# Optimization experiments

Measured on AMD Instinct MI355X. Metric: run time of the kernel, lower is better.

Reference implementation:

```python
import jax, jax.numpy as jnp
import numpy as np

N = 20000      # nodes
E = 640000     # edges
DIN = 92       # atom feature dim
C = 128        # hidden_dim
H = 2          # GAT heads
LAYERS = 2     # shared-weight layer count
BN_EPS = 1e-5


def _bn(x, gamma, beta):
    # BatchNorm1d in training mode: batch statistics over the node axis
    mu = x.mean(0)
    var = x.var(0)
    return (x - mu) * jax.lax.rsqrt(var + BN_EPS) * gamma + beta


def _segment_softmax(logits, seg, num_segments):
    # logits: [E', H], seg: [E'] destination ids; softmax per destination node
    m = jax.ops.segment_max(logits, seg, num_segments=num_segments)
    ex = jnp.exp(logits - m[seg])
    s = jax.ops.segment_sum(ex, seg, num_segments=num_segments)
    return ex / s[seg]


def setup_inputs() -> dict:
    key = jax.random.key(0)
    ks = jax.random.split(key, 16)
    def w(k, shape, fan_in):
        return (jax.random.normal(k, shape, jnp.float32) / np.sqrt(fan_in)).astype(jnp.float32)
    return {
        "node_features_s": jax.random.normal(ks[0], (N, DIN), jnp.float32),
        "edge_index_s": jax.random.randint(ks[1], (2, E), 0, N, dtype=jnp.int64),
        "eps_noise": jax.random.normal(ks[2], (N, C), jnp.float32),
        # atom_emb: Linear(DIN,C) + BN + ReLU
        "W_emb": w(ks[3], (DIN, C), DIN), "b_emb": jnp.zeros((C,), jnp.float32),
        "g_emb": jnp.ones((C,), jnp.float32), "be_emb": jnp.zeros((C,), jnp.float32),
        # GIN MLP (shared across all enc layers): Linear+BN+ReLU+Linear
        "W1": w(ks[4], (C, C), C), "b1": jnp.zeros((C,), jnp.float32),
        "g1": jnp.ones((C,), jnp.float32), "be1": jnp.zeros((C,), jnp.float32),
        "W2": w(ks[5], (C, C), C), "b2": jnp.zeros((C,), jnp.float32),
        # VAE heads
        "W_mu": w(ks[6], (C, C), C), "b_mu": jnp.zeros((C,), jnp.float32),
        "W_var": w(ks[7], (C, C), C), "b_var": jnp.zeros((C,), jnp.float32),
        # GAT (shared across all dec layers): lin -> [N,H,C], attention vecs, bias
        "W_gat": w(ks[8], (C, H * C), C),
        "att_src": w(ks[9], (H, C), C), "att_dst": w(ks[10], (H, C), C),
        "b_gat": jnp.zeros((H * C,), jnp.float32),
        # decoder Linear(H*C, C)
        "W_dec": w(ks[11], (H * C, C), H * C), "b_dec": jnp.zeros((C,), jnp.float32),
    }


def reference(node_features_s, edge_index_s, eps_noise,
              W_emb, b_emb, g_emb, be_emb,
              W1, b1, g1, be1, W2, b2,
              W_mu, b_mu, W_var, b_var,
              W_gat, att_src, att_dst, b_gat,
              W_dec, b_dec):
    src, dst = edge_index_s[0], edge_index_s[1]

    # atom embedding
    x = jax.nn.relu(_bn(node_features_s @ W_emb + b_emb, g_emb, be_emb))

    # GIN encoder (eps=0, sum aggregation), shared weights across layers
    for _ in range(LAYERS):
        agg = jax.ops.segment_sum(x[src], dst, num_segments=N)
        h = x + agg
        h = jax.nn.relu(_bn(h @ W1 + b1, g1, be1))
        x = h @ W2 + b2

    mu = x @ W_mu + b_mu
    logvar = x @ W_var + b_var
    z = eps_noise * jnp.exp(0.5 * logvar) + mu
    zin = z

    # GAT decoder with self-loops (PyG default), shared weights
    loop = jnp.arange(N, dtype=src.dtype)
    src_sl = jnp.concatenate([src, loop])
    dst_sl = jnp.concatenate([dst, loop])
    zout = z
    for _ in range(LAYERS):
        hh = (zout @ W_gat).reshape(N, H, C)            # [N,H,C]
        a_s = jnp.einsum('nhc,hc->nh', hh, att_src)     # [N,H]
        a_d = jnp.einsum('nhc,hc->nh', hh, att_dst)
        logits = jax.nn.leaky_relu(a_s[src_sl] + a_d[dst_sl], 0.2)  # [E',H]
        alpha = _segment_softmax(logits, dst_sl, N)
        msg = alpha[:, :, None] * hh[src_sl]            # [E',H,C]
        out = jax.ops.segment_sum(msg, dst_sl, num_segments=N)      # [N,H,C]
        out = out.reshape(N, H * C) + b_gat
        zout = out @ W_dec + b_dec

    return (zin, zout, mu, logvar)
```

## Files before the change

### kernel.cpp

```cpp
#include <hip/hip_runtime.h>
#include <hip/hip_bf16.h>

#define NN   20000
#define DIN_ 92
#define CC   128
#define EE   640000
#define CAP  128
#define BN_EPS 1e-5f

typedef short short8 __attribute__((ext_vector_type(8)));
typedef float floatx4 __attribute__((ext_vector_type(4)));

static __device__ __forceinline__ float b2f(__hip_bfloat16 v) { return __bfloat162float(v); }
static __device__ __forceinline__ float ldf(const void* p, int i, int f32) {
    return f32 ? ((const float*)p)[i]
               : __bfloat162float(((const __hip_bfloat16*)p)[i]);
}
static __device__ __forceinline__ void stf(void* p, int i, float v, int f32) {
    if (f32) ((float*)p)[i] = v;
    else     ((__hip_bfloat16*)p)[i] = __float2bfloat16(v);
}
static __device__ __forceinline__ float leaky02(float x) { return x > 0.f ? x : 0.2f * x; }

static __device__ __forceinline__ float2 bfp(unsigned w) {
    return make_float2(__uint_as_float(w << 16), __uint_as_float(w & 0xffff0000u));
}
static __device__ __forceinline__ float4 bf4(unsigned x, unsigned y) {
    return make_float4(__uint_as_float(x << 16), __uint_as_float(x & 0xffff0000u),
                       __uint_as_float(y << 16), __uint_as_float(y & 0xffff0000u));
}
static __device__ __forceinline__ uint2 f4bf(float4 v) {
    union { uint2 u; __hip_bfloat16 b[4]; } x;
    x.b[0] = __float2bfloat16(v.x); x.b[1] = __float2bfloat16(v.y);
    x.b[2] = __float2bfloat16(v.z); x.b[3] = __float2bfloat16(v.w);
    return x.u;
}
static __device__ __forceinline__ unsigned f2bf(float2 v) {
    union { unsigned u; __hip_bfloat16 b[2]; } x;
    x.b[0] = __float2bfloat16(v.x); x.b[1] = __float2bfloat16(v.y);
    return x.u;
}
static __device__ __forceinline__ short bf16s(float v) {
    union { __hip_bfloat16 b; unsigned short u; } cv;
    cv.b = __float2bfloat16(v);
    return (short)cv.u;
}

#define R0_ 12288
#define R1_ (R0_ + 16384)
#define R2_ (R1_ + 16384)
#define R3_ (R2_ + 16384)
#define R4_ (R3_ + 16384)
#define R5_ (R4_ + 32768)
#define R6_ (R5_ + 32768)
#define TCVT (R6_ + NN * 96)
#define CHUNK 2048
#define NCH ((EE + CHUNK - 1) / CHUNK)
#define HB (NCH * 8)
#define CVTB ((TCVT + 255) / 256)

__global__ __launch_bounds__(256) void cvt_scatter_kernel(
    const void* __restrict__ w_emb, const void* __restrict__ w1,
    const void* __restrict__ w2, const void* __restrict__ wmu,
    const void* __restrict__ wvar, const void* __restrict__ wgat,
    const void* __restrict__ wdec, const void* __restrict__ xin,
    const unsigned* __restrict__ ei,
    __hip_bfloat16* __restrict__ dst,
    int* __restrict__ flags, int* __restrict__ deg,
    unsigned short* __restrict__ csr)
{
    if ((int)blockIdx.x < HB) {
        __shared__ int cz;
        if (threadIdx.x == 0) cz = 0;
        __syncthreads();
        if (ei[2 * threadIdx.x + 1] == 0u) atomicAdd(&cz, 1);
        __syncthreads();
        const int i64 = (cz >= 250);
        int r = blockIdx.x & 7;
        int c = blockIdx.x >> 3;
        int base = c * CHUNK + threadIdx.x;
#pragma unroll
        for (int k = 0; k < CHUNK / 256; k++) {
            int e = base + k * 256;
            if (e < EE) {
                int d = i64 ? (int)((const long long*)ei)[EE + e] : ((const int*)ei)[EE + e];
                if (d / 2500 == r) {
                    int s = i64 ? (int)((const long long*)ei)[e] : ((const int*)ei)[e];
                    int pos = atomicAdd(&deg[d], 1);
                    if (pos < CAP) csr[(d << 7) + pos] = (unsigned short)s;
                }
            }
        }
        return;
    }

    __shared__ int cnt_band, cnt_zero;
    if (threadIdx.x == 0) { cnt_band = 0; cnt_zero = 0; }
    __syncthreads();
    {
        unsigned wv = ((const unsigned*)xin)[threadIdx.x];
        unsigned eb = ((wv & 0xFFFFu) >> 7) & 0xFFu;
        if (eb >= 90u && eb <= 140u) atomicAdd(&cnt_band, 1);
        if ((int)blockIdx.x == HB && ei[2 * threadIdx.x + 1] == 0u) atomicAdd(&cnt_zero, 1);
    }
    __syncthreads();
    const int f32 = (cnt_band < 200) ? 1 : 0;
    if ((int)blockIdx.x == HB && threadIdx.x == 0) {
        flags[0] = f32;
        flags[1] = (cnt_zero >= 250) ? 1 : 0;
    }

    int i = ((int)blockIdx.x - HB) * 256 + threadIdx.x;
    if (i >= TCVT) return;
    float v;
    if (i < R0_) {
        int n = i / 96, k = i - n * 96;
        v = (k < DIN_) ? ldf(w_emb, k * 128 + n, f32) : 0.f;
    } else if (i < R1_) {
        int j = i - R0_; int n = j >> 7, k = j & 127; v = ldf(w1, k * 128 + n, f32);
    } else if (i < R2_) {
        int j = i - R1_; int n = j >> 7, k = j & 127; v = ldf(w2, k * 128 + n, f32);
    } else if (i < R3_) {
        int j = i - R2_; int n = j >> 7, k = j & 127; v = ldf(wmu, k * 128 + n, f32);
    } else if (i < R4_) {
        int j = i - R3_; int n = j >> 7, k = j & 127; v = ldf(wvar, k * 128 + n, f32);
    } else if (i < R5_) {
        int j = i - R4_; int n = j >> 7, k = j & 127; v = ldf(wgat, k * 256 + n, f32);
    } else if (i < R6_) {
        int j = i - R5_; int n = j >> 8, k = j & 255; v = ldf(wdec, k * 128 + n, f32);
    } else {
        int j = i - R6_; int row = j / 96, k = j - row * 96;
        v = (k < DIN_) ? ldf(xin, row * DIN_ + k, f32) : 0.f;
    }
    dst[i] = __float2bfloat16(v);
}

template<int KP, int NC, int CG, int OUT_MODE, int STATS, int BN_A>
__global__ __launch_bounds__(256) void mfma_gemm_kernel(
    const __hip_bfloat16* __restrict__ A,
    const __hip_bfloat16* __restrict__ WT,
    const void* __restrict__ bias,
    void* __restrict__ Cout, int out_off, float* __restrict__ part,
    const float* __restrict__ bnsums, const void* __restrict__ bng,
    const void* __restrict__ bnbe, const int* __restrict__ flags)
{
    const int f32 = flags[0];
    constexpr int MB = 16 * (4 / CG);
    constexpr int CT = NC / (16 * CG);
    __shared__ float sc_s[128], sh_s[128];
    if (BN_A) {
        int t = threadIdx.x;
        if (t < 128) {
            float mean = bnsums[t] * (1.f / NN);
            float var  = bnsums[128 + t] * (1.f / NN) - mean * mean;
            float rs   = rsqrtf(fmaxf(var, 0.f) + BN_EPS);
            float g    = ldf(bng, t, f32);
            float sc   = rs * g;
            sc_s[t] = sc;
            sh_s[t] = ldf(bnbe, t, f32) - mean * sc;
        }
        __syncthreads();
    }
    int w = threadIdx.x >> 6, l = threadIdx.x & 63;
    int rt = w / CG, cg = w - rt * CG;
    int m0 = blockIdx.x * MB + rt * 16;
    int n0 = cg * (16 * CT);
    int l15 = l & 15, kq = (l >> 4) * 8;
    const __hip_bfloat16* arow = A + (size_t)(m0 + l15) * KP + kq;

    floatx4 acc[CT];
#pragma unroll
    for (int ct = 0; ct < CT; ct++) acc[ct] = (floatx4){0.f, 0.f, 0.f, 0.f};

    for (int kc = 0; kc < KP / 32; kc++) {
        short8 a = *(const short8*)(arow + kc * 32);
        if (BN_A) {
#pragma unroll
            for (int k = 0; k < 8; k++) {
                int c = kq + kc * 32 + k;
                float v = __uint_as_float(((unsigned)(unsigned short)a[k]) << 16);
                float o = v * sc_s[c] + sh_s[c];
                a[k] = bf16s(o > 0.f ? o : 0.f);
            }
        }
#pragma unroll
        for (int ct = 0; ct < CT; ct++) {
            const __hip_bfloat16* brow = WT + (size_t)(n0 + ct * 16 + l15) * KP + kq;
            short8 b = *(const short8*)(brow + kc * 32);
            acc[ct] = __builtin_amdgcn_mfma_f32_16x16x32_bf16(a, b, acc[ct], 0, 0, 0);
        }
    }

    int quad = l >> 4;
#pragma unroll
    for (int ct = 0; ct < CT; ct++) {
        int col = n0 + ct * 16 + l15;
        float bb = bias ? ldf(bias, col, f32) : 0.f;
        float sl = 0.f, ql = 0.f;
#pragma unroll
        for (int r = 0; r < 4; r++) {
            int row = m0 + quad * 4 + r;
            float v = acc[ct][r] + bb;
            size_t o = (size_t)row * NC + col;
            if (OUT_MODE == 0)      ((float*)Cout)[o] = v;
            else if (OUT_MODE == 1) ((__hip_bfloat16*)Cout)[o] = __float2bfloat16(v);
            else                    stf(Cout, out_off + (int)o, v, f32);
            if (STATS) { sl += v; ql += v * v; }
        }
        if (STATS) {
            sl += __shfl_xor(sl, 16); sl += __shfl_xor(sl, 32);
            ql += __shfl_xor(ql, 16); ql += __shfl_xor(ql, 32);
            if (quad == 0) {
                part[blockIdx.x * 512 + rt * 256 + col] = sl;
                part[blockIdx.x * 512 + rt * 256 + 128 + col] = ql;
            }
        }
    }
}

__global__ void bn_reduce_kernel(const float* __restrict__ part, float* __restrict__ sums,
                                 int nblk)
{
    int c = threadIdx.x;
    int per = (nblk + (int)gridDim.x - 1) / (int)gridDim.x;
    int b0 = blockIdx.x * per;
    int b1 = min(b0 + per, nblk);
    float v = 0.f;
    for (int b = b0; b < b1; b++)
        v += part[b * 512 + c] + part[b * 512 + 256 + c];
    atomicAdd(&sums[c], v);
}

__global__ __launch_bounds__(256) void gemm_zatt_kernel(
    const __hip_bfloat16* __restrict__ A, const __hip_bfloat16* __restrict__ WTmuv,
    const __hip_bfloat16* __restrict__ WTgat,
    const void* __restrict__ eps, const void* __restrict__ b_mu, const void* __restrict__ b_var,
    __hip_bfloat16* __restrict__ HH,
    const void* __restrict__ attS, const void* __restrict__ attD,
    float* __restrict__ AS, float* __restrict__ AD,
    void* __restrict__ out, const int* __restrict__ flags)
{
    const int f32 = flags[0];
    __shared__ float zs[16][257];
    __shared__ __hip_bfloat16 zb[16][136];
    __shared__ float sS[4][16], sD[4][16];
    int w = threadIdx.x >> 6, l = threadIdx.x & 63;
    int m0 = blockIdx.x * 16;
    int n0 = w * 64;
    int l15 = l & 15, quad = l >> 4, kq = quad * 8;
    const __hip_bfloat16* arow = A + (size_t)(m0 + l15) * 128 + kq;

    floatx4 acc[4];
#pragma unroll
    for (int ct = 0; ct < 4; ct++) acc[ct] = (floatx4){0.f, 0.f, 0.f, 0.f};
    for (int kc = 0; kc < 4; kc++) {
        short8 a = *(const short8*)(arow + kc * 32);
#pragma unroll
        for (int ct = 0; ct < 4; ct++) {
            const __hip_bfloat16* brow = WTmuv + (size_t)(n0 + ct * 16 + l15) * 128 + kq;
            short8 b = *(const short8*)(brow + kc * 32);
            acc[ct] = __builtin_amdgcn_mfma_f32_16x16x32_bf16(a, b, acc[ct], 0, 0, 0);
        }
    }
#pragma unroll
    for (int ct = 0; ct < 4; ct++) {
#pragma unroll
        for (int r = 0; r < 4; r++)
            zs[quad * 4 + r][n0 + ct * 16 + l15] = acc[ct][r];
    }
    __syncthreads();
    int t = threadIdx.x;
    const int NB2 = NN * CC;
#pragma unroll
    for (int k = 0; k < 8; k++) {
        int idx = k * 256 + t;
        int row = idx >> 7, c = idx & 127;
        float mu = zs[row][c]       + ldf(b_mu,  c, f32);
        float lv = zs[row][128 + c] + ldf(b_var, c, f32);
        int gi = (m0 + row) * 128 + c;
        float z = ldf(eps, gi, f32) * expf(0.5f * lv) + mu;
        zb[row][c] = __float2bfloat16(z);
        stf(out, gi, z, f32);
        stf(out, 2 * NB2 + gi, mu, f32);
        stf(out, 3 * NB2 + gi, lv, f32);
    }
    __syncthreads();

    int h = w >> 1;
    floatx4 acc2[4];
#pragma unroll
    for (int ct = 0; ct < 4; ct++) acc2[ct] = (floatx4){0.f, 0.f, 0.f, 0.f};
    for (int kc = 0; kc < 4; kc++) {
        short8 a = *(const short8*)(&zb[l15][kq + kc * 32]);
#pragma unroll
        for (int ct = 0; ct < 4; ct++) {
            const __hip_bfloat16* brow = WTgat + (size_t)(n0 + ct * 16 + l15) * 128 + kq;
            short8 b = *(const short8*)(brow + kc * 32);
            acc2[ct] = __builtin_amdgcn_mfma_f32_16x16x32_bf16(a, b, acc2[ct], 0, 0, 0);
        }
    }
    float spart[4] = {0.f, 0.f, 0.f, 0.f};
    float dpart[4] = {0.f, 0.f, 0.f, 0.f};
#pragma unroll
    for (int ct = 0; ct < 4; ct++) {
        int col = n0 + ct * 16 + l15;
        int cm  = col - 128 * h;
        float as_w = ldf(attS, h * CC + cm, f32);
        float ad_w = ldf(attD, h * CC + cm, f32);
#pragma unroll
        for (int r = 0; r < 4; r++) {
            float v = acc2[ct][r];
            HH[(size_t)(m0 + quad * 4 + r) * 256 + col] = __float2bfloat16(v);
            spart[r] += v * as_w;
            dpart[r] += v * ad_w;
        }
    }
#pragma unroll
    for (int o = 1; o <= 8; o <<= 1) {
#pragma unroll
        for (int r = 0; r < 4; r++) {
            spart[r] += __shfl_xor(spart[r], o);
            dpart[r] += __shfl_xor(dpart[r], o);
        }
    }
    if (l15 == 0) {
#pragma unroll
        for (int r = 0; r < 4; r++) {
            sS[w][quad * 4 + r] = spart[r];
            sD[w][quad * 4 + r] = dpart[r];
        }
    }
    __syncthreads();
    if (t < 32) {
        int row = t & 15, hh2 = t >> 4;
        AS[(m0 + row) * 2 + hh2] = sS[2 * hh2][row] + sS[2 * hh2 + 1][row];
        AD[(m0 + row) * 2 + hh2] = sD[2 * hh2][row] + sD[2 * hh2 + 1][row];
    }
}

__global__ __launch_bounds__(256) void gemm_decatt_kernel(
    const __hip_bfloat16* __restrict__ A, const __hip_bfloat16* __restrict__ WTdec,
    const __hip_bfloat16* __restrict__ WTgat, const void* __restrict__ b_dec,
    __hip_bfloat16* __restrict__ HH,
    const void* __restrict__ attS, const void* __restrict__ attD,
    float* __restrict__ AS, float* __restrict__ AD, const int* __restrict__ flags)
{
    const int f32 = flags[0];
    __shared__ __hip_bfloat16 zo[32][136];
    int w = threadIdx.x >> 6, l = threadIdx.x & 63;
    int rt = w >> 1, cg = w & 1;
    int l15 = l & 15, quad = l >> 4, kq = quad * 8;
    int m0 = blockIdx.x * 32;

    {
        int n0 = cg * 64;
        const __hip_bfloat16* arow = A + (size_t)(m0 + rt * 16 + l15) * 256 + kq;
        floatx4 acc[4];
#pragma unroll
        for (int ct = 0; ct < 4; ct++) acc[ct] = (floatx4){0.f, 0.f, 0.f, 0.f};
        for (int kc = 0; kc < 8; kc++) {
            short8 a = *(const short8*)(arow + kc * 32);
#pragma unroll
            for (int ct = 0; ct < 4; ct++) {
                const __hip_bfloat16* brow = WTdec + (size_t)(n0 + ct * 16 + l15) * 256 + kq;
                short8 b = *(const short8*)(brow + kc * 32);
                acc[ct] = __builtin_amdgcn_mfma_f32_16x16x32_bf16(a, b, acc[ct], 0, 0, 0);
            }
        }
#pragma unroll
        for (int ct = 0; ct < 4; ct++) {
            int col = n0 + ct * 16 + l15;
            float bb = ldf(b_dec, col, f32);
#pragma unroll
            for (int r = 0; r < 4; r++)
                zo[rt * 16 + quad * 4 + r][col] = __float2bfloat16(acc[ct][r] + bb);
        }
    }
    __syncthreads();

    int n0 = cg * 128;
    floatx4 acc2[8];
#pragma unroll
    for (int ct = 0; ct < 8; ct++) acc2[ct] = (floatx4){0.f, 0.f, 0.f, 0.f};
    for (int kc = 0; kc < 4; kc++) {
        short8 a = *(const short8*)(&zo[rt * 16 + l15][kq + kc * 32]);
#pragma unroll
        for (int ct = 0; ct < 8; ct++) {
            const __hip_bfloat16* brow = WTgat + (size_t)(n0 + ct * 16 + l15) * 128 + kq;
            short8 b = *(const short8*)(brow + kc * 32);
            acc2[ct] = __builtin_amdgcn_mfma_f32_16x16x32_bf16(a, b, acc2[ct], 0, 0, 0);
        }
    }
    float spart[4] = {0.f, 0.f, 0.f, 0.f};
    float dpart[4] = {0.f, 0.f, 0.f, 0.f};
#pragma unroll
    for (int ct = 0; ct < 8; ct++) {
        int cm  = ct * 16 + l15;
        int col = n0 + cm;
        float as_w = ldf(attS, cg * CC + cm, f32);
        float ad_w = ldf(attD, cg * CC + cm, f32);
#pragma unroll
        for (int r = 0; r < 4; r++) {
            float v = acc2[ct][r];
            HH[(size_t)(m0 + rt * 16 + quad * 4 + r) * 256 + col] = __float2bfloat16(v);
            spart[r] += v * as_w;
            dpart[r] += v * ad_w;
        }
    }
#pragma unroll
    for (int o = 1; o <= 8; o <<= 1) {
#pragma unroll
        for (int r = 0; r < 4; r++) {
            spart[r] += __shfl_xor(spart[r], o);
            dpart[r] += __shfl_xor(dpart[r], o);
        }
    }
    if (l15 == 0) {
#pragma unroll
        for (int r = 0; r < 4; r++) {
            int row = m0 + rt * 16 + quad * 4 + r;
            AS[row * 2 + cg] = spart[r];
            AD[row * 2 + cg] = dpart[r];
        }
    }
}

__global__ __launch_bounds__(256) void gat_fused_kernel(
    const uint2* __restrict__ HH2,
    const float* __restrict__ AS, const float* __restrict__ AD,
    const int* __restrict__ deg, const unsigned short* __restrict__ csr,
    const void* __restrict__ b_gat, __hip_bfloat16* __restrict__ ALPHA,
    uint2* __restrict__ OUT2, const int* __restrict__ flags)
{
    const int f32 = flags[0];
    int d = (blockIdx.x * blockDim.x + threadIdx.x) >> 6;
    int l = threadIdx.x & 63;
    if (d >= NN) return;
    int h = l >> 5, j = l & 31;
    int b = d << 7;
    int e = b + min(deg[d], CAP);
    float adh = AD[d * 2 + h];
    float self_e = expf(leaky02(AS[d * 2 + h] + adh));
    __hip_bfloat16* __restrict__ AH = ALPHA + (size_t)h * (NN * CAP);

    float sum = (j == 0) ? self_e : 0.f;
    for (int i = b + j; i < e; i += 32) {
        float ex = expf(leaky02(AS[(int)csr[i] * 2 + h] + adh));
        __hip_bfloat16 exb = __float2bfloat16(ex);
        AH[i] = exb;
        sum += __bfloat162float(exb);
    }
#pragma unroll
    for (int o = 16; o; o >>= 1) sum += __shfl_xor(sum, o);
    float inv = 1.f / sum;

    uint2 wv = HH2[(size_t)d * 64 + l];
    float4 p = bf4(wv.x, wv.y);
    float4 acc = make_float4(self_e * p.x, self_e * p.y, self_e * p.z, self_e * p.w);
    int i = b;
    for (; i + 8 <= e; i += 8) {
        int s0 = csr[i],     s1 = csr[i + 1], s2 = csr[i + 2], s3 = csr[i + 3];
        int s4 = csr[i + 4], s5 = csr[i + 5], s6 = csr[i + 6], s7 = csr[i + 7];
        float a1 = b2f(AH[i]),     a2 = b2f(AH[i + 1]), a3 = b2f(AH[i + 2]), a4 = b2f(AH[i + 3]);
        float a5 = b2f(AH[i + 4]), a6 = b2f(AH[i + 5]), a7 = b2f(AH[i + 6]), a8 = b2f(AH[i + 7]);
        uint2 w0 = HH2[(size_t)s0 * 64 + l];
        uint2 w1 = HH2[(size_t)s1 * 64 + l];
        uint2 w2 = HH2[(size_t)s2 * 64 + l];
        uint2 w3 = HH2[(size_t)s3 * 64 + l];
        uint2 w4 = HH2[(size_t)s4 * 64 + l];
        uint2 w5 = HH2[(size_t)s5 * 64 + l];
        uint2 w6 = HH2[(size_t)s6 * 64 + l];
        uint2 w7 = HH2[(size_t)s7 * 64 + l];
        float4 f;
        f = bf4(w0.x, w0.y); acc.x += a1 * f.x; acc.y += a1 * f.y; acc.z += a1 * f.z; acc.w += a1 * f.w;
        f = bf4(w1.x, w1.y); acc.x += a2 * f.x; acc.y += a2 * f.y; acc.z += a2 * f.z; acc.w += a2 * f.w;
        f = bf4(w2.x, w2.y); acc.x += a3 * f.x; acc.y += a3 * f.y; acc.z += a3 * f.z; acc.w += a3 * f.w;
        f = bf4(w3.x, w3.y); acc.x += a4 * f.x; acc.y += a4 * f.y; acc.z += a4 * f.z; acc.w += a4 * f.w;
        f = bf4(w4.x, w4.y); acc.x += a5 * f.x; acc.y += a5 * f.y; acc.z += a5 * f.z; acc.w += a5 * f.w;
        f = bf4(w5.x, w5.y); acc.x += a6 * f.x; acc.y += a6 * f.y; acc.z += a6 * f.z; acc.w += a6 * f.w;
        f = bf4(w6.x, w6.y); acc.x += a7 * f.x; acc.y += a7 * f.y; acc.z += a7 * f.z; acc.w += a7 * f.w;
        f = bf4(w7.x, w7.y); acc.x += a8 * f.x; acc.y += a8 * f.y; acc.z += a8 * f.z; acc.w += a8 * f.w;
    }
    for (; i + 4 <= e; i += 4) {
        int s0 = csr[i], s1 = csr[i + 1], s2 = csr[i + 2], s3 = csr[i + 3];
        float a1 = b2f(AH[i]), a2 = b2f(AH[i + 1]), a3 = b2f(AH[i + 2]), a4 = b2f(AH[i + 3]);
        uint2 w0 = HH2[(size_t)s0 * 64 + l];
        uint2 w1 = HH2[(size_t)s1 * 64 + l];
        uint2 w2 = HH2[(size_t)s2 * 64 + l];
        uint2 w3 = HH2[(size_t)s3 * 64 + l];
        float4 f;
        f = bf4(w0.x, w0.y); acc.x += a1 * f.x; acc.y += a1 * f.y; acc.z += a1 * f.z; acc.w += a1 * f.w;
        f = bf4(w1.x, w1.y); acc.x += a2 * f.x; acc.y += a2 * f.y; acc.z += a2 * f.z; acc.w += a2 * f.w;
        f = bf4(w2.x, w2.y); acc.x += a3 * f.x; acc.y += a3 * f.y; acc.z += a3 * f.z; acc.w += a3 * f.w;
        f = bf4(w3.x, w3.y); acc.x += a4 * f.x; acc.y += a4 * f.y; acc.z += a4 * f.z; acc.w += a4 * f.w;
    }
    for (; i < e; i++) {
        int s = csr[i];
        float al = b2f(AH[i]);
        uint2 wq = HH2[(size_t)s * 64 + l];
        float4 f = bf4(wq.x, wq.y);
        acc.x += al * f.x; acc.y += al * f.y; acc.z += al * f.z; acc.w += al * f.w;
    }
    int c0 = 4 * l;
    acc.x = acc.x * inv + ldf(b_gat, c0 + 0, f32);
    acc.y = acc.y * inv + ldf(b_gat, c0 + 1, f32);
    acc.z = acc.z * inv + ldf(b_gat, c0 + 2, f32);
    acc.w = acc.w * inv + ldf(b_gat, c0 + 3, f32);
    OUT2[(size_t)d * 64 + l] = f4bf(acc);
}

#define BNR4(f) do { if (BN_A) { \
    f.x = fmaxf(f.x * sc0 + sh0, 0.f); \
    f.y = fmaxf(f.y * sc1 + sh1, 0.f); \
    f.z = fmaxf(f.z * sc2 + sh2, 0.f); \
    f.w = fmaxf(f.w * sc3 + sh3, 0.f); } } while (0)

template<int BN_A>
__global__ __launch_bounds__(256) void gin_gather_kernel(
    const uint2* __restrict__ X2, uint2* __restrict__ H2,
    const int* __restrict__ deg, const unsigned short* __restrict__ csr,
    const float* __restrict__ sums, const void* __restrict__ g,
    const void* __restrict__ be, const int* __restrict__ flags)
{
    int hw = (blockIdx.x * blockDim.x + threadIdx.x) >> 5;
    int l5 = threadIdx.x & 31;
    if (hw >= NN) return;
    float sc0 = 0.f, sc1 = 0.f, sc2 = 0.f, sc3 = 0.f;
    float sh0 = 0.f, sh1 = 0.f, sh2 = 0.f, sh3 = 0.f;
    if (BN_A) {
        const int f32 = flags[0];
        int c = 4 * l5;
        float m0 = sums[c + 0] * (1.f / NN), m1 = sums[c + 1] * (1.f / NN);
        float m2 = sums[c + 2] * (1.f / NN), m3 = sums[c + 3] * (1.f / NN);
        float v0 = sums[128 + c + 0] * (1.f / NN) - m0 * m0;
        float v1 = sums[128 + c + 1] * (1.f / NN) - m1 * m1;
        float v2 = sums[128 + c + 2] * (1.f / NN) - m2 * m2;
        float v3 = sums[128 + c + 3] * (1.f / NN) - m3 * m3;
        sc0 = rsqrtf(fmaxf(v0, 0.f) + BN_EPS) * ldf(g, c + 0, f32);
        sc1 = rsqrtf(fmaxf(v1, 0.f) + BN_EPS) * ldf(g, c + 1, f32);
        sc2 = rsqrtf(fmaxf(v2, 0.f) + BN_EPS) * ldf(g, c + 2, f32);
        sc3 = rsqrtf(fmaxf(v3, 0.f) + BN_EPS) * ldf(g, c + 3, f32);
        sh0 = ldf(be, c + 0, f32) - m0 * sc0;
        sh1 = ldf(be, c + 1, f32) - m1 * sc1;
        sh2 = ldf(be, c + 2, f32) - m2 * sc2;
        sh3 = ldf(be, c + 3, f32) - m3 * sc3;
    }
    int d = hw;
    uint2 w0 = X2[(size_t)d * 32 + l5];
    float4 acc = bf4(w0.x, w0.y);
    BNR4(acc);
    int b = d << 7;
    int e = b + min(deg[d], CAP);
    int i = b;
    for (; i + 4 <= e; i += 4) {
        int s0 = csr[i], s1 = csr[i + 1], s2 = csr[i + 2], s3 = csr[i + 3];
        uint2 a0 = X2[(size_t)s0 * 32 + l5];
        uint2 a1 = X2[(size_t)s1 * 32 + l5];
        uint2 a2 = X2[(size_t)s2 * 32 + l5];
        uint2 a3 = X2[(size_t)s3 * 32 + l5];
        float4 f0 = bf4(a0.x, a0.y), f1 = bf4(a1.x, a1.y);
        float4 f2 = bf4(a2.x, a2.y), f3 = bf4(a3.x, a3.y);
        BNR4(f0); BNR4(f1); BNR4(f2); BNR4(f3);
        acc.x += f0.x + f1.x + f2.x + f3.x;
        acc.y += f0.y + f1.y + f2.y + f3.y;
        acc.z += f0.z + f1.z + f2.z + f3.z;
        acc.w += f0.w + f1.w + f2.w + f3.w;
    }
    for (; i < e; i++) {
        uint2 a = X2[(size_t)csr[i] * 32 + l5];
        float4 f = bf4(a.x, a.y);
        BNR4(f);
        acc.x += f.x; acc.y += f.y; acc.z += f.z; acc.w += f.w;
    }
    H2[(size_t)d * 32 + l5] = f4bf(acc);
}

extern "C" void kernel_launch(void* const* d_in, const int* in_sizes, int n_in,
                              void* d_out, int out_size, void* d_ws, size_t ws_size,
                              hipStream_t stream)
{
    const void* xin    = d_in[0];
    const void* ei     = d_in[1];
    const void* eps    = d_in[2];
    const void* W_emb  = d_in[3];
    const void* b_emb  = d_in[4];
    const void* g_emb  = d_in[5];
    const void* be_emb = d_in[6];
    const void* W1     = d_in[7];
    const void* b1     = d_in[8];
    const void* g1     = d_in[9];
    const void* be1    = d_in[10];
    const void* W2     = d_in[11];
    const void* b2     = d_in[12];
    const void* W_mu   = d_in[13];
    const void* b_mu   = d_in[14];
    const void* W_var  = d_in[15];
    const void* b_var  = d_in[16];
    const void* W_gat  = d_in[17];
    const void* attS   = d_in[18];
    const void* attD   = d_in[19];
    const void* b_gat  = d_in[20];
    const void* W_dec  = d_in[21];
    const void* b_dec  = d_in[22];

    float* ws = (float*)d_ws;
    const size_t NB = (size_t)NN * CC;
    float* B0 = ws;
    float* B1 = ws + 1 * NB;
    float* B2 = ws + 2 * NB;
    __hip_bfloat16* Xbf   = (__hip_bfloat16*)B2;
    __hip_bfloat16* Hbf   = Xbf + NB;
    __hip_bfloat16* HHbf  = (__hip_bfloat16*)B0;
    __hip_bfloat16* OUTbf = (__hip_bfloat16*)B1;
    __hip_bfloat16* Ybf   = (__hip_bfloat16*)B1;
    float* TAIL = ws + 4 * NB;
    float* AS      = TAIL;
    float* AD      = TAIL + 40000;
    int*   FLAGS   = (int*)(TAIL + 80000);
    float* SUMSALL = (float*)(FLAGS + 16);
    int*   DEG     = (int*)(SUMSALL + 768);
    float* PART    = (float*)(DEG + 20000);
    unsigned short* CSR16 = (unsigned short*)(PART + 320000);
    __hip_bfloat16* ALPHAb = (__hip_bfloat16*)((float*)(PART + 320000) + NN * CAP / 2);
    __hip_bfloat16* WTB = (__hip_bfloat16*)((float*)(PART + 320000) + NN * CAP / 2 + NN * CAP);
    __hip_bfloat16* WTemb = WTB;
    __hip_bfloat16* WT1   = WTB + R0_;
    __hip_bfloat16* WT2   = WTB + R1_;
    __hip_bfloat16* WTmuv = WTB + R2_;
    __hip_bfloat16* WTgat = WTB + R4_;
    __hip_bfloat16* WTdec = WTB + R5_;
    __hip_bfloat16* Xin   = WTB + R6_;

    const int GEMM_BLKS = NN / 32;

    hipMemsetAsync(SUMSALL, 0, (768 + 20000) * sizeof(int), stream);

    cvt_scatter_kernel<<<HB + CVTB, 256, 0, stream>>>(
        W_emb, W1, W2, W_mu, W_var, W_gat, W_dec, xin,
        (const unsigned*)ei, WTB, FLAGS, DEG, CSR16);

    mfma_gemm_kernel<96, 128, 2, 1, 1, 0><<<GEMM_BLKS, 256, 0, stream>>>(
        Xin, WTemb, b_emb, Ybf, 0, PART, nullptr, nullptr, nullptr, FLAGS);
    bn_reduce_kernel<<<8, 256, 0, stream>>>(PART, SUMSALL, GEMM_BLKS);

    for (int t = 0; t < 2; t++) {
        float* SUMS_T = SUMSALL + 256 * (1 + t);
        if (t == 0) {
            gin_gather_kernel<1><<<NN / 8, 256, 0, stream>>>(
                (const uint2*)Ybf, (uint2*)Hbf, DEG, CSR16,
                SUMSALL, g_emb, be_emb, FLAGS);
        } else {
            gin_gather_kernel<0><<<NN / 8, 256, 0, stream>>>(
                (const uint2*)Xbf, (uint2*)Hbf, DEG, CSR16,
                nullptr, nullptr, nullptr, FLAGS);
        }
        mfma_gemm_kernel<128, 128, 2, 1, 1, 0><<<GEMM_BLKS, 256, 0, stream>>>(
            Hbf, WT1, b1, Ybf, 0, PART, nullptr, nullptr, nullptr, FLAGS);
        bn_reduce_kernel<<<8, 256, 0, stream>>>(PART, SUMS_T, GEMM_BLKS);
        mfma_gemm_kernel<128, 128, 2, 1, 0, 1><<<GEMM_BLKS, 256, 0, stream>>>(
            Ybf, WT2, b2, Xbf, 0, nullptr, SUMS_T, g1, be1, FLAGS);
    }

    gemm_zatt_kernel<<<NN / 16, 256, 0, stream>>>(
        Xbf, WTmuv, WTgat, eps, b_mu, b_var, HHbf, attS, attD, AS, AD, d_out, FLAGS);
    gat_fused_kernel<<<(NN * 64) / 256, 256, 0, stream>>>(
        (const uint2*)HHbf, AS, AD, DEG, CSR16, b_gat, ALPHAb, (uint2*)OUTbf, FLAGS);

    gemm_decatt_kernel<<<GEMM_BLKS, 256, 0, stream>>>(
        OUTbf, WTdec, WTgat, b_dec, HHbf, attS, attD, AS, AD, FLAGS);
    gat_fused_kernel<<<(NN * 64) / 256, 256, 0, stream>>>(
        (const uint2*)HHbf, AS, AD, DEG, CSR16, b_gat, ALPHAb, (uint2*)OUTbf, FLAGS);

    mfma_gemm_kernel<256, 128, 2, 2, 0, 0><<<GEMM_BLKS, 256, 0, stream>>>(
        OUTbf, WTdec, b_dec, d_out, NN * CC, nullptr, nullptr, nullptr, nullptr, FLAGS);
}
```

Baseline: 489.9 us.

## Fuse GIN neighbor gather with first MLP GEMM via shared-memory tile

Replaces the separate GIN gather kernel plus first GEMM with a single kernel. Each block gathers and sums neighbor rows for 16 nodes into an LDS tile, then multiplies that tile by W1 with MFMA and writes BN partial statistics. This removes the write and re-read of the aggregated H buffer and one launch per layer. In exchange, the GEMM blocks are smaller (16 rows) with B loaded from global, there are twice as many partial-stat blocks, and the workspace layout shifts to fit the larger PART buffer.

```diff
diff --git a/kernel.cpp b/kernel.cpp
--- a/kernel.cpp
+++ b/kernel.cpp
@@ -214,6 +214,123 @@
                 part[blockIdx.x * 512 + rt * 256 + col] = sl;
                 part[blockIdx.x * 512 + rt * 256 + 128 + col] = ql;
             }
+        }
+    }
+}
+
+template<int BN_A>
+__global__ __launch_bounds__(256) void gemm_gin_kernel(
+    const uint2* __restrict__ X2, const __hip_bfloat16* __restrict__ WT,
+    const void* __restrict__ bias, __hip_bfloat16* __restrict__ Cout,
+    float* __restrict__ part,
+    const int* __restrict__ deg, const unsigned short* __restrict__ csr,
+    const float* __restrict__ bnsums, const void* __restrict__ bng,
+    const void* __restrict__ bnbe, const int* __restrict__ flags)
+{
+    const int f32 = flags[0];
+    __shared__ __hip_bfloat16 ab[16][136];
+    __shared__ float sc_s[128], sh_s[128];
+    int t = threadIdx.x;
+    if (BN_A) {
+        if (t < 128) {
+            float mean = bnsums[t] * (1.f / NN);
+            float var  = bnsums[128 + t] * (1.f / NN) - mean * mean;
+            float rs   = rsqrtf(fmaxf(var, 0.f) + BN_EPS);
+            float g    = ldf(bng, t, f32);
+            float sc   = rs * g;
+            sc_s[t] = sc;
+            sh_s[t] = ldf(bnbe, t, f32) - mean * sc;
+        }
+        __syncthreads();
+    }
+    int m0 = blockIdx.x * 16;
+
+    int hwl = t >> 5;
+    int l5  = t & 31;
+    int c4  = 4 * l5;
+    float sc0 = 0.f, sc1 = 0.f, sc2 = 0.f, sc3 = 0.f;
+    float sh0 = 0.f, sh1 = 0.f, sh2 = 0.f, sh3 = 0.f;
+    if (BN_A) {
+        sc0 = sc_s[c4 + 0]; sc1 = sc_s[c4 + 1]; sc2 = sc_s[c4 + 2]; sc3 = sc_s[c4 + 3];
+        sh0 = sh_s[c4 + 0]; sh1 = sh_s[c4 + 1]; sh2 = sh_s[c4 + 2]; sh3 = sh_s[c4 + 3];
+    }
+#define GBNR(f) do { if (BN_A) { \
+    f.x = fmaxf(f.x * sc0 + sh0, 0.f); \
+    f.y = fmaxf(f.y * sc1 + sh1, 0.f); \
+    f.z = fmaxf(f.z * sc2 + sh2, 0.f); \
+    f.w = fmaxf(f.w * sc3 + sh3, 0.f); } } while (0)
+#pragma unroll
+    for (int q = 0; q < 2; q++) {
+        int row = hwl * 2 + q;
+        int d = m0 + row;
+        uint2 w0 = X2[(size_t)d * 32 + l5];
+        float4 acc = bf4(w0.x, w0.y);
+        GBNR(acc);
+        int b = d << 7;
+        int e = b + min(deg[d], CAP);
+        int i = b;
+        for (; i + 4 <= e; i += 4) {
+            int s0 = csr[i], s1 = csr[i + 1], s2 = csr[i + 2], s3 = csr[i + 3];
+            uint2 a0 = X2[(size_t)s0 * 32 + l5];
+            uint2 a1 = X2[(size_t)s1 * 32 + l5];
+            uint2 a2 = X2[(size_t)s2 * 32 + l5];
+            uint2 a3 = X2[(size_t)s3 * 32 + l5];
+            float4 f0 = bf4(a0.x, a0.y), f1 = bf4(a1.x, a1.y);
+            float4 f2 = bf4(a2.x, a2.y), f3 = bf4(a3.x, a3.y);
+            GBNR(f0); GBNR(f1); GBNR(f2); GBNR(f3);
+            acc.x += f0.x + f1.x + f2.x + f3.x;
+            acc.y += f0.y + f1.y + f2.y + f3.y;
+            acc.z += f0.z + f1.z + f2.z + f3.z;
+            acc.w += f0.w + f1.w + f2.w + f3.w;
+        }
+        for (; i < e; i++) {
+            uint2 a = X2[(size_t)csr[i] * 32 + l5];
+            float4 f = bf4(a.x, a.y);
+            GBNR(f);
+            acc.x += f.x; acc.y += f.y; acc.z += f.z; acc.w += f.w;
+        }
+        ab[row][c4 + 0] = __float2bfloat16(acc.x);
+        ab[row][c4 + 1] = __float2bfloat16(acc.y);
+        ab[row][c4 + 2] = __float2bfloat16(acc.z);
+        ab[row][c4 + 3] = __float2bfloat16(acc.w);
+    }
+#undef GBNR
+    __syncthreads();
+
+    int w = t >> 6, l = t & 63;
+    int n0 = w * 32;
+    int l15 = l & 15, quad = l >> 4, kq = quad * 8;
+    floatx4 acc[2];
+    acc[0] = (floatx4){0.f, 0.f, 0.f, 0.f};
+    acc[1] = (floatx4){0.f, 0.f, 0.f, 0.f};
+    for (int kc = 0; kc < 4; kc++) {
+        short8 a = *(const short8*)(&ab[l15][kq + kc * 32]);
+#pragma unroll
+        for (int ct = 0; ct < 2; ct++) {
+            const __hip_bfloat16* brow = WT + (size_t)(n0 + ct * 16 + l15) * 128 + kq;
+            short8 b = *(const short8*)(brow + kc * 32);
+            acc[ct] = __builtin_amdgcn_mfma_f32_16x16x32_bf16(a, b, acc[ct], 0, 0, 0);
+        }
+    }
+#pragma unroll
+    for (int ct = 0; ct < 2; ct++) {
+        int col = n0 + ct * 16 + l15;
+        float bb = ldf(bias, col, f32);
+        float sl = 0.f, ql = 0.f;
+#pragma unroll
+        for (int r = 0; r < 4; r++) {
+            int row = m0 + quad * 4 + r;
+            float v = acc[ct][r] + bb;
+            Cout[(size_t)row * 128 + col] = __float2bfloat16(v);
+            sl += v; ql += v * v;
+        }
+        sl += __shfl_xor(sl, 16); sl += __shfl_xor(sl, 32);
+        ql += __shfl_xor(ql, 16); ql += __shfl_xor(ql, 32);
+        if (quad == 0) {
+            part[blockIdx.x * 512 + col] = sl;
+            part[blockIdx.x * 512 + 128 + col] = ql;
+            part[blockIdx.x * 512 + 256 + col] = 0.f;
+            part[blockIdx.x * 512 + 384 + col] = 0.f;
         }
     }
 }
@@ -507,72 +624,6 @@
     acc.z = acc.z * inv + ldf(b_gat, c0 + 2, f32);
     acc.w = acc.w * inv + ldf(b_gat, c0 + 3, f32);
     OUT2[(size_t)d * 64 + l] = f4bf(acc);
-}
-
-#define BNR4(f) do { if (BN_A) { \
-    f.x = fmaxf(f.x * sc0 + sh0, 0.f); \
-    f.y = fmaxf(f.y * sc1 + sh1, 0.f); \
-    f.z = fmaxf(f.z * sc2 + sh2, 0.f); \
-    f.w = fmaxf(f.w * sc3 + sh3, 0.f); } } while (0)
-
-template<int BN_A>
-__global__ __launch_bounds__(256) void gin_gather_kernel(
-    const uint2* __restrict__ X2, uint2* __restrict__ H2,
-    const int* __restrict__ deg, const unsigned short* __restrict__ csr,
-    const float* __restrict__ sums, const void* __restrict__ g,
-    const void* __restrict__ be, const int* __restrict__ flags)
-{
-    int hw = (blockIdx.x * blockDim.x + threadIdx.x) >> 5;
-    int l5 = threadIdx.x & 31;
-    if (hw >= NN) return;
-    float sc0 = 0.f, sc1 = 0.f, sc2 = 0.f, sc3 = 0.f;
-    float sh0 = 0.f, sh1 = 0.f, sh2 = 0.f, sh3 = 0.f;
-    if (BN_A) {
-        const int f32 = flags[0];
-        int c = 4 * l5;
-        float m0 = sums[c + 0] * (1.f / NN), m1 = sums[c + 1] * (1.f / NN);
-        float m2 = sums[c + 2] * (1.f / NN), m3 = sums[c + 3] * (1.f / NN);
-        float v0 = sums[128 + c + 0] * (1.f / NN) - m0 * m0;
-        float v1 = sums[128 + c + 1] * (1.f / NN) - m1 * m1;
-        float v2 = sums[128 + c + 2] * (1.f / NN) - m2 * m2;
-        float v3 = sums[128 + c + 3] * (1.f / NN) - m3 * m3;
-        sc0 = rsqrtf(fmaxf(v0, 0.f) + BN_EPS) * ldf(g, c + 0, f32);
-        sc1 = rsqrtf(fmaxf(v1, 0.f) + BN_EPS) * ldf(g, c + 1, f32);
-        sc2 = rsqrtf(fmaxf(v2, 0.f) + BN_EPS) * ldf(g, c + 2, f32);
-        sc3 = rsqrtf(fmaxf(v3, 0.f) + BN_EPS) * ldf(g, c + 3, f32);
-        sh0 = ldf(be, c + 0, f32) - m0 * sc0;
-        sh1 = ldf(be, c + 1, f32) - m1 * sc1;
-        sh2 = ldf(be, c + 2, f32) - m2 * sc2;
-        sh3 = ldf(be, c + 3, f32) - m3 * sc3;
-    }
-    int d = hw;
-    uint2 w0 = X2[(size_t)d * 32 + l5];
-    float4 acc = bf4(w0.x, w0.y);
-    BNR4(acc);
-    int b = d << 7;
-    int e = b + min(deg[d], CAP);
-    int i = b;
-    for (; i + 4 <= e; i += 4) {
-        int s0 = csr[i], s1 = csr[i + 1], s2 = csr[i + 2], s3 = csr[i + 3];
-        uint2 a0 = X2[(size_t)s0 * 32 + l5];
-        uint2 a1 = X2[(size_t)s1 * 32 + l5];
-        uint2 a2 = X2[(size_t)s2 * 32 + l5];
-        uint2 a3 = X2[(size_t)s3 * 32 + l5];
-        float4 f0 = bf4(a0.x, a0.y), f1 = bf4(a1.x, a1.y);
-        float4 f2 = bf4(a2.x, a2.y), f3 = bf4(a3.x, a3.y);
-        BNR4(f0); BNR4(f1); BNR4(f2); BNR4(f3);
-        acc.x += f0.x + f1.x + f2.x + f3.x;
-        acc.y += f0.y + f1.y + f2.y + f3.y;
-        acc.z += f0.z + f1.z + f2.z + f3.z;
-        acc.w += f0.w + f1.w + f2.w + f3.w;
-    }
-    for (; i < e; i++) {
-        uint2 a = X2[(size_t)csr[i] * 32 + l5];
-        float4 f = bf4(a.x, a.y);
-        BNR4(f);
-        acc.x += f.x; acc.y += f.y; acc.z += f.z; acc.w += f.w;
-    }
-    H2[(size_t)d * 32 + l5] = f4bf(acc);
 }
 
 extern "C" void kernel_launch(void* const* d_in, const int* in_sizes, int n_in,
@@ -620,9 +671,9 @@
     float* SUMSALL = (float*)(FLAGS + 16);
     int*   DEG     = (int*)(SUMSALL + 768);
     float* PART    = (float*)(DEG + 20000);
-    unsigned short* CSR16 = (unsigned short*)(PART + 320000);
-    __hip_bfloat16* ALPHAb = (__hip_bfloat16*)((float*)(PART + 320000) + NN * CAP / 2);
-    __hip_bfloat16* WTB = (__hip_bfloat16*)((float*)(PART + 320000) + NN * CAP / 2 + NN * CAP);
+    unsigned short* CSR16 = (unsigned short*)(PART + 640000);
+    __hip_bfloat16* ALPHAb = (__hip_bfloat16*)((float*)(PART + 640000) + NN * CAP / 2);
+    __hip_bfloat16* WTB = (__hip_bfloat16*)((float*)(PART + 640000) + NN * CAP / 2 + NN * CAP);
     __hip_bfloat16* WTemb = WTB;
     __hip_bfloat16* WT1   = WTB + R0_;
     __hip_bfloat16* WT2   = WTB + R1_;
@@ -643,23 +694,18 @@
         Xin, WTemb, b_emb, Ybf, 0, PART, nullptr, nullptr, nullptr, FLAGS);
     bn_reduce_kernel<<<8, 256, 0, stream>>>(PART, SUMSALL, GEMM_BLKS);
 
-    for (int t = 0; t < 2; t++) {
-        float* SUMS_T = SUMSALL + 256 * (1 + t);
-        if (t == 0) {
-            gin_gather_kernel<1><<<NN / 8, 256, 0, stream>>>(
-                (const uint2*)Ybf, (uint2*)Hbf, DEG, CSR16,
-                SUMSALL, g_emb, be_emb, FLAGS);
-        } else {
-            gin_gather_kernel<0><<<NN / 8, 256, 0, stream>>>(
-                (const uint2*)Xbf, (uint2*)Hbf, DEG, CSR16,
-                nullptr, nullptr, nullptr, FLAGS);
-        }
-        mfma_gemm_kernel<128, 128, 2, 1, 1, 0><<<GEMM_BLKS, 256, 0, stream>>>(
-            Hbf, WT1, b1, Ybf, 0, PART, nullptr, nullptr, nullptr, FLAGS);
-        bn_reduce_kernel<<<8, 256, 0, stream>>>(PART, SUMS_T, GEMM_BLKS);
-        mfma_gemm_kernel<128, 128, 2, 1, 0, 1><<<GEMM_BLKS, 256, 0, stream>>>(
-            Ybf, WT2, b2, Xbf, 0, nullptr, SUMS_T, g1, be1, FLAGS);
-    }
+    gemm_gin_kernel<1><<<NN / 16, 256, 0, stream>>>(
+        (const uint2*)Ybf, WT1, b1, Hbf, PART, DEG, CSR16,
+        SUMSALL, g_emb, be_emb, FLAGS);
+    bn_reduce_kernel<<<8, 256, 0, stream>>>(PART, SUMSALL + 256, NN / 16);
+    mfma_gemm_kernel<128, 128, 2, 1, 0, 1><<<GEMM_BLKS, 256, 0, stream>>>(
+        Hbf, WT2, b2, Xbf, 0, nullptr, SUMSALL + 256, g1, be1, FLAGS);
+    gemm_gin_kernel<0><<<NN / 16, 256, 0, stream>>>(
+        (const uint2*)Xbf, WT1, b1, Ybf, PART, DEG, CSR16,
+        nullptr, nullptr, nullptr, FLAGS);
+    bn_reduce_kernel<<<8, 256, 0, stream>>>(PART, SUMSALL + 512, NN / 16);
+    mfma_gemm_kernel<128, 128, 2, 1, 0, 1><<<GEMM_BLKS, 256, 0, stream>>>(
+        Ybf, WT2, b2, Xbf, 0, nullptr, SUMSALL + 512, g1, be1, FLAGS);
 
     gemm_zatt_kernel<<<NN / 16, 256, 0, stream>>>(
         Xbf, WTmuv, WTgat, eps, b_mu, b_var, HHbf, attS, attD, AS, AD, d_out, FLAGS);
```

Measured after the change: 512.6 us. 1.05x slower.
